# Optimization experiments

Measured on AMD Instinct MI355X. Metric: run time of the kernel, lower is better.

## Reference

```python
import jax, jax.numpy as jnp
import numpy as np

BN_EPS = 1e-5


def _bn_train(x, gamma, beta):
    # torch BatchNorm1d in training mode: normalize with batch mean and
    # biased batch variance.
    mu = jnp.mean(x, axis=0)
    var = jnp.var(x, axis=0)
    return (x - mu) * jax.lax.rsqrt(var + BN_EPS) * gamma + beta


def setup_inputs() -> dict:
    key = jax.random.key(0)
    ks = jax.random.split(key, 12)
    N, F_D, F_C, E, VOCAB, H = 16384, 26, 10, 16, 200000, 400
    D_IN = (F_D + F_C) * E  # 576
    return {
        "Xi_dense": jax.random.normal(ks[0], (N, F_D, 1), jnp.float32),
        "Xv": jax.random.uniform(ks[1], (N, F_D + F_C), jnp.float32),
        "Wd": jax.random.normal(ks[2], (F_D, E), jnp.float32) * 0.1,
        "bd": jax.random.normal(ks[3], (F_D, E), jnp.float32) * 0.1,
        "tables": jax.random.normal(ks[4], (F_C, VOCAB, E), jnp.float32) * 0.1,
        "W1": jax.random.normal(ks[5], (H, D_IN), jnp.float32) * 0.05,
        "b1": jax.random.normal(ks[6], (H,), jnp.float32) * 0.05,
        "g1": jnp.ones((H,), jnp.float32),
        "be1": jnp.zeros((H,), jnp.float32),
        "W2": jax.random.normal(ks[7], (H, H), jnp.float32) * 0.05,
        "b2": jax.random.normal(ks[8], (H,), jnp.float32) * 0.05,
        "g2": jnp.ones((H,), jnp.float32),
        "be2": jnp.zeros((H,), jnp.float32),
        "bias_vec": jax.random.normal(ks[9], (N,), jnp.float32),
        "Xi_cat": jax.random.randint(ks[10], (N, F_C, 1), 0, VOCAB, jnp.int32),
    }


def reference(Xi_dense, Xv, Wd, bd, tables, W1, b1, g1, be1,
              W2, b2, g2, be2, bias_vec, Xi_cat):
    N = Xi_dense.shape[0]
    # dense fields: per-field Linear(1, E) -> x * W + b, shape (N, 26, E)
    dense_emb = Xi_dense * Wd[None] + bd[None]  # (N,26,1)*(1,26,E) broadcast
    # categorical fields: per-field embedding lookup, shape (N, 10, E)
    cat_emb = jax.vmap(lambda tbl, idx: tbl[idx], in_axes=(0, 1), out_axes=1)(
        tables, Xi_cat[:, :, 0])
    # scale each field embedding by its Xv value
    all_emb = jnp.concatenate([dense_emb, cat_emb], axis=1) * Xv[:, :, None]  # (N,36,E)

    # fm first order: concat of all scaled field embeddings
    fm_first = all_emb.reshape(N, -1)  # (N, 576)
    # fm second order: 0.5 * ((sum)^2 - sum of squares)
    s = jnp.sum(all_emb, axis=1)                       # (N, E)
    fm_second = 0.5 * (s * s - jnp.sum(all_emb * all_emb, axis=1))  # (N, E)

    # deep part: Linear -> BatchNorm (train-mode stats) per hidden layer;
    # dropout p=0 -> identity.
    deep = fm_first
    deep = _bn_train(deep @ W1.T + b1, g1, be1)
    deep = _bn_train(deep @ W2.T + b2, g2, be2)

    total = (jnp.sum(fm_first, axis=1) + jnp.sum(fm_second, axis=1)
             + jnp.sum(deep, axis=1) + bias_vec)
    return total
```

## Files before the change

### kernel.cpp

```cpp
#include <hip/hip_runtime.h>

#define BN_EPS 1e-5f

typedef unsigned short u16;
typedef __attribute__((ext_vector_type(8))) short bf16x8;
typedef __attribute__((ext_vector_type(4))) float f32x4;

__device__ __forceinline__ u16 f2bf(float x) {
  union { float f; unsigned int u; } v; v.f = x;
  unsigned int r = v.u + 0x7fffu + ((v.u >> 16) & 1u);
  return (u16)(r >> 16);
}
__device__ __forceinline__ float bf2f(u16 h) {
  union { unsigned int u; float f; } v; v.u = ((unsigned int)h) << 16;
  return v.f;
}

__device__ __forceinline__ float wave_reduce_sum(float v) {
#pragma unroll
  for (int off = 1; off < 64; off <<= 1) v += __shfl_xor(v, off, 64);
  return v;
}

__device__ __forceinline__ void gload_lds16(const void* g, void* l) {
  __builtin_amdgcn_global_load_lds(
      (const __attribute__((address_space(1))) void*)g,
      (__attribute__((address_space(3))) void*)l, 16, 0, 0);
}

#define NBE 4096
__global__ __launch_bounds__(256) void embed_prep(
    const float* __restrict__ Xi_dense, const float* __restrict__ Xv,
    const float* __restrict__ Wd, const float* __restrict__ bd,
    const float* __restrict__ tables, const int* __restrict__ Xi_cat,
    const float* __restrict__ bias_vec, const float* __restrict__ W1,
    u16* __restrict__ fm_first, float* __restrict__ partial,
    u16* __restrict__ W1h) {
  const int t = threadIdx.x;
  if (blockIdx.x >= NBE) {
    const int base = (blockIdx.x - NBE) * 4096;
#pragma unroll
    for (int e = 0; e < 16; ++e) {
      const int idx = base + e * 256 + t;
      const int r = idx / 576;
      const int j = idx - r * 576;
      W1h[idx] = (r < 400) ? f2bf(W1[r * 576 + j]) : (u16)0;
    }
    return;
  }
  const int lane = t & 63;
  const int n = blockIdx.x * 4 + (t >> 6);

  const float* xv = Xv + n * 36;
  float sum_all = 0.f, s_e = 0.f, q_e = 0.f;

#pragma unroll
  for (int k = 0; k < 9; ++k) {
    const int idx = lane + 64 * k;
    const int f = idx >> 4;
    const int e = idx & 15;
    float val;
    if (f < 26) {
      val = Xi_dense[n * 26 + f] * Wd[f * 16 + e] + bd[f * 16 + e];
    } else {
      const int fc = f - 26;
      const int row = Xi_cat[n * 10 + fc];
      val = tables[(size_t)fc * 200000 * 16 + (size_t)row * 16 + e];
    }
    val *= xv[f];
    fm_first[(size_t)n * 576 + idx] = f2bf(val);
    sum_all += val;
    s_e += val;
    q_e += val * val;
  }

  float s_tot = s_e;
  s_tot += __shfl_xor(s_tot, 16, 64);
  s_tot += __shfl_xor(s_tot, 32, 64);
  float q_tot = q_e;
  q_tot += __shfl_xor(q_tot, 16, 64);
  q_tot += __shfl_xor(q_tot, 32, 64);

  const float fm2 = 0.5f * (s_tot * s_tot - q_tot);
  const float red1 = wave_reduce_sum(sum_all);
  const float red2 = wave_reduce_sum(fm2) * 0.25f;
  if (lane == 0) partial[n] = red1 + red2 + bias_vec[n];
}

template <int NFR>
__device__ __forceinline__ void gemm_body(
    const u16* __restrict__ A, int lda, const u16* __restrict__ W, int ldw,
    const float* __restrict__ bias, int nbias, u16* __restrict__ Y, int ldc,
    int Ncap, float* __restrict__ pS, float* __restrict__ pQ, int K, int nxb,
    int bx, int by, u16* As, u16* Bs, float (&rS)[2][4][2][16],
    float (&rQ)[2][4][2][16]) {
  const int t = threadIdx.x;
  const int bm = bx * 64;
  const int bn = by * 128;
  const int wid = t >> 6, lane = t & 63;
  const int wr = wid >> 1, wc = wid & 1;
  const int lr = lane & 15, lk = (lane >> 4) * 8;
  const int sr = lane >> 2;
  const int sk = (lane & 3) * 8;
  const bool active = (NFR == 4) || (wc == 0);

  f32x4 acc[2][NFR] = {};

  for (int kt = 0; kt < K; kt += 32) {
    gload_lds16(&A[(size_t)(bm + wid * 16 + sr) * lda + kt + sk],
                &As[wid * 512]);
#pragma unroll
    for (int i = 0; i < 2; ++i) {
      const int c = wid * 2 + i;
      if (NFR == 4 || c < 2)
        gload_lds16(&W[(size_t)(bn + c * 16 + sr) * ldw + kt + sk],
                    &Bs[c * 512]);
    }
    __syncthreads();

    if (active) {
      bf16x8 af[2], bfv[NFR];
#pragma unroll
      for (int mf = 0; mf < 2; ++mf)
        af[mf] = *(const bf16x8*)&As[(wr * 32 + mf * 16 + lr) * 32 + lk];
#pragma unroll
      for (int nf = 0; nf < NFR; ++nf)
        bfv[nf] = *(const bf16x8*)&Bs[(wc * 64 + nf * 16 + lr) * 32 + lk];
#pragma unroll
      for (int mf = 0; mf < 2; ++mf)
#pragma unroll
        for (int nf = 0; nf < NFR; ++nf)
          acc[mf][nf] = __builtin_amdgcn_mfma_f32_16x16x32_bf16(
              af[mf], bfv[nf], acc[mf][nf], 0, 0, 0);
    }
    __syncthreads();
  }

  const int l4 = (lane >> 4) * 4;
  if (active) {
#pragma unroll
    for (int nf = 0; nf < NFR; ++nf) {
      const int col = bn + wc * 64 + nf * 16 + lr;
      const float bb = (col < nbias) ? bias[col] : 0.f;
      float s = 0.f, q = 0.f;
#pragma unroll
      for (int mf = 0; mf < 2; ++mf) {
#pragma unroll
        for (int r = 0; r < 4; ++r) {
          const int row = bm + wr * 32 + mf * 16 + l4 + r;
          const float v = acc[mf][nf][r] + bb;
          s += v;
          q += v * v;
          if (col < Ncap) Y[(size_t)row * ldc + col] = f2bf(v);
        }
      }
      s += __shfl_xor(s, 16, 64);
      s += __shfl_xor(s, 32, 64);
      q += __shfl_xor(q, 16, 64);
      q += __shfl_xor(q, 32, 64);
      if (lane < 16) {
        rS[wc][nf][wr][lr] = s;
        rQ[wc][nf][wr][lr] = q;
      }
    }
  }
  __syncthreads();
  if (t < (NFR == 4 ? 128 : 32)) {
    const int wcc = t >> 6, nff = (t >> 4) & 3, c = t & 15;
    pS[(size_t)(bn + t) * nxb + bx] =
        rS[wcc][nff][0][c] + rS[wcc][nff][1][c];
    pQ[(size_t)(bn + t) * nxb + bx] =
        rQ[wcc][nff][0][c] + rQ[wcc][nff][1][c];
  }
}

__global__ __launch_bounds__(256) void gemm_bf16(
    const u16* __restrict__ A, int lda,
    const u16* __restrict__ W, int ldw,
    const float* __restrict__ bias, int nbias,
    u16* __restrict__ Y, int ldc, int Ncap,
    float* __restrict__ pS, float* __restrict__ pQ, int K, int nxb) {
  __shared__ u16 As[64 * 32];
  __shared__ u16 Bs[128 * 32];
  __shared__ float rS[2][4][2][16];
  __shared__ float rQ[2][4][2][16];
  const int bid = blockIdx.x;
  const int l = (bid & 7) * (gridDim.x >> 3) + (bid >> 3);
  const int bx = l >> 2, by = l & 3;
  if (by < 3)
    gemm_body<4>(A, lda, W, ldw, bias, nbias, Y, ldc, Ncap, pS, pQ, K, nxb,
                 bx, by, As, Bs, rS, rQ);
  else
    gemm_body<2>(A, lda, W, ldw, bias, nbias, Y, ldc, Ncap, pS, pQ, K, nxb,
                 bx, by, As, Bs, rS, rQ);
}

__global__ __launch_bounds__(256) void bn_ac(
    const float* __restrict__ pS, const float* __restrict__ pQ,
    const float* __restrict__ g, const float* __restrict__ be,
    float* __restrict__ a, float* __restrict__ c, int nxb) {
  const int wid = threadIdx.x >> 6, lane = threadIdx.x & 63;
  const int col = blockIdx.x * 4 + wid;
  float S = 0.f, Q = 0.f;
  for (int i = lane; i < nxb; i += 64) {
    S += pS[(size_t)col * nxb + i];
    Q += pQ[(size_t)col * nxb + i];
  }
#pragma unroll
  for (int off = 1; off < 64; off <<= 1) {
    S += __shfl_xor(S, off, 64);
    Q += __shfl_xor(Q, off, 64);
  }
  if (lane == 0) {
    const float mu = S * (1.f / 16384.f);
    const float var = Q * (1.f / 16384.f) - mu * mu;
    const float aa = g[col] * rsqrtf(var + BN_EPS);
    a[col] = aa;
    c[col] = be[col] - mu * aa;
  }
}

__global__ __launch_bounds__(256) void prep2(
    const float* __restrict__ a1, const float* __restrict__ c1,
    const float* __restrict__ W2, const float* __restrict__ b2,
    u16* __restrict__ W2p, float* __restrict__ b2p) {
  const int t = threadIdx.x;
  const int lane = t & 63;
  const int row = blockIdx.x * 4 + (t >> 6);
  const ushort4 z4 = {0, 0, 0, 0};
  if (row >= 400) {
    const int j1 = lane * 4;
    *(ushort4*)&W2p[(size_t)row * 416 + j1] = z4;
    const int j2 = 256 + lane * 4;
    if (j2 < 416) *(ushort4*)&W2p[(size_t)row * 416 + j2] = z4;
    if (lane == 0) b2p[row] = 0.f;
    return;
  }
  float dot = 0.f;
  {
    const int j = lane * 4;
    const float4 w = *(const float4*)&W2[(size_t)row * 400 + j];
    const float4 la = *(const float4*)&a1[j];
    const float4 lc = *(const float4*)&c1[j];
    ushort4 o = {f2bf(w.x * la.x), f2bf(w.y * la.y), f2bf(w.z * la.z),
                 f2bf(w.w * la.w)};
    *(ushort4*)&W2p[(size_t)row * 416 + j] = o;
    dot += w.x * lc.x + w.y * lc.y + w.z * lc.z + w.w * lc.w;
  }
  {
    const int j = 256 + lane * 4;
    if (j < 400) {
      const float4 w = *(const float4*)&W2[(size_t)row * 400 + j];
      const float4 la = *(const float4*)&a1[j];
      const float4 lc = *(const float4*)&c1[j];
      ushort4 o = {f2bf(w.x * la.x), f2bf(w.y * la.y), f2bf(w.z * la.z),
                   f2bf(w.w * la.w)};
      *(ushort4*)&W2p[(size_t)row * 416 + j] = o;
      dot += w.x * lc.x + w.y * lc.y + w.z * lc.z + w.w * lc.w;
    } else if (j < 416) {
      *(ushort4*)&W2p[(size_t)row * 416 + j] = z4;
    }
  }
  dot = wave_reduce_sum(dot);
  if (lane == 0) b2p[row] = b2[row] + dot;
}

__global__ __launch_bounds__(256) void final_kernel(
    const u16* __restrict__ Y2, const float* __restrict__ a2,
    const float* __restrict__ c2, const float* __restrict__ partial,
    float* __restrict__ out) {
  const int t = threadIdx.x;
  const int lane = t & 63;
  const int wid = t >> 6;
  const int j0 = lane * 8;
  float ar[8], cr[8];
  if (j0 < 400) {
    const float4 a0 = *(const float4*)&a2[j0];
    const float4 a1v = *(const float4*)&a2[j0 + 4];
    const float4 c0 = *(const float4*)&c2[j0];
    const float4 c1v = *(const float4*)&c2[j0 + 4];
    ar[0] = a0.x; ar[1] = a0.y; ar[2] = a0.z; ar[3] = a0.w;
    ar[4] = a1v.x; ar[5] = a1v.y; ar[6] = a1v.z; ar[7] = a1v.w;
    cr[0] = c0.x; cr[1] = c0.y; cr[2] = c0.z; cr[3] = c0.w;
    cr[4] = c1v.x; cr[5] = c1v.y; cr[6] = c1v.z; cr[7] = c1v.w;
  } else {
#pragma unroll
    for (int k = 0; k < 8; ++k) { ar[k] = 0.f; cr[k] = 0.f; }
  }
#pragma unroll
  for (int r = 0; r < 4; ++r) {
    const int n = blockIdx.x * 16 + wid * 4 + r;
    float acc = 0.f;
    if (j0 < 400) {
      const bf16x8 y = *(const bf16x8*)&Y2[(size_t)n * 400 + j0];
#pragma unroll
      for (int k = 0; k < 8; ++k)
        acc += fmaf(ar[k], bf2f((u16)y[k]), cr[k]);
    }
    acc = wave_reduce_sum(acc);
    if (lane == 0) out[n] = partial[n] + acc;
  }
}

extern "C" void kernel_launch(void* const* d_in, const int* in_sizes, int n_in,
                              void* d_out, int out_size, void* d_ws,
                              size_t ws_size, hipStream_t stream) {
  const float* Xi_dense = (const float*)d_in[0];
  const float* Xv = (const float*)d_in[1];
  const float* Wd = (const float*)d_in[2];
  const float* bd = (const float*)d_in[3];
  const float* tables = (const float*)d_in[4];
  const float* W1 = (const float*)d_in[5];
  const float* b1 = (const float*)d_in[6];
  const float* g1 = (const float*)d_in[7];
  const float* be1 = (const float*)d_in[8];
  const float* W2 = (const float*)d_in[9];
  const float* b2 = (const float*)d_in[10];
  const float* g2 = (const float*)d_in[11];
  const float* be2 = (const float*)d_in[12];
  const float* bias_vec = (const float*)d_in[13];
  const int* Xi_cat = (const int*)d_in[14];

  constexpr int N = 16384;
  constexpr int DIN = 576;
  constexpr int H = 400;
  constexpr int KP = 416;
  constexpr int WPAD = 512;
  constexpr int NXB = 256;

  u16* fm_first = (u16*)d_ws;
  u16* Y1h = fm_first + (size_t)N * DIN;
  u16* Y2h = Y1h + (size_t)N * KP;
  u16* W1h = Y2h + (size_t)N * H;
  u16* W2p = W1h + (size_t)WPAD * DIN;
  float* fptr = (float*)(W2p + (size_t)WPAD * KP);
  float* partial = fptr;
  float* pS = partial + N;
  float* pQ = pS + WPAD * NXB;
  float* a1 = pQ + WPAD * NXB;
  float* c1 = a1 + WPAD;
  float* a2 = c1 + WPAD;
  float* c2 = a2 + WPAD;
  float* b2p = c2 + WPAD;

  embed_prep<<<NBE + 72, 256, 0, stream>>>(Xi_dense, Xv, Wd, bd, tables,
                                           Xi_cat, bias_vec, W1, fm_first,
                                           partial, W1h);

  gemm_bf16<<<NXB * 4, 256, 0, stream>>>(fm_first, DIN, W1h, DIN, b1, H,
                                         Y1h, KP, KP, pS, pQ, DIN, NXB);

  bn_ac<<<100, 256, 0, stream>>>(pS, pQ, g1, be1, a1, c1, NXB);
  prep2<<<128, 256, 0, stream>>>(a1, c1, W2, b2, W2p, b2p);

  gemm_bf16<<<NXB * 4, 256, 0, stream>>>(Y1h, KP, W2p, KP, b2p, H,
                                         Y2h, H, H, pS, pQ, KP, NXB);

  bn_ac<<<100, 256, 0, stream>>>(pS, pQ, g2, be2, a2, c2, NXB);

  final_kernel<<<N / 16, 256, 0, stream>>>(Y2h, a2, c2, partial,
                                           (float*)d_out);
}
```

Baseline: 67.88 us.

## Double-buffer LDS in GEMM and enlarge M tile to 128 rows

The bf16 MFMA GEMM now uses double-buffered LDS tiles, loading the next K-slice while computing the current one, with one barrier per iteration instead of two. The M tile grows from 64 to 128 rows, so each wave computes 4 M fragments and the number of row blocks (NXB) halves. MFMA sections are wrapped in s_setprio to favour issue. The aim is to hide global-load latency and raise data reuse per block. The cost is more LDS and accumulator registers, which can lower occupancy, and half as many blocks in the grid.

```diff
diff --git a/kernel.cpp b/kernel.cpp
--- a/kernel.cpp
+++ b/kernel.cpp
@@ -92,10 +92,10 @@
     const u16* __restrict__ A, int lda, const u16* __restrict__ W, int ldw,
     const float* __restrict__ bias, int nbias, u16* __restrict__ Y, int ldc,
     int Ncap, float* __restrict__ pS, float* __restrict__ pQ, int K, int nxb,
-    int bx, int by, u16* As, u16* Bs, float (&rS)[2][4][2][16],
-    float (&rQ)[2][4][2][16]) {
+    int bx, int by, u16 (*As)[128 * 32], u16 (*Bs)[128 * 32],
+    float (&rS)[2][4][2][16], float (&rQ)[2][4][2][16]) {
   const int t = threadIdx.x;
-  const int bm = bx * 64;
+  const int bm = bx * 128;
   const int bn = by * 128;
   const int wid = t >> 6, lane = t & 63;
   const int wr = wid >> 1, wc = wid & 1;
@@ -104,37 +104,53 @@
   const int sk = (lane & 3) * 8;
   const bool active = (NFR == 4) || (wc == 0);
 
-  f32x4 acc[2][NFR] = {};
-
-  for (int kt = 0; kt < K; kt += 32) {
-    gload_lds16(&A[(size_t)(bm + wid * 16 + sr) * lda + kt + sk],
-                &As[wid * 512]);
+  f32x4 acc[4][NFR] = {};
+
+  auto STAGE = [&](int buf, int kt) {
 #pragma unroll
     for (int i = 0; i < 2; ++i) {
       const int c = wid * 2 + i;
+      gload_lds16(&A[(size_t)(bm + c * 16 + sr) * lda + kt + sk],
+                  &As[buf][c * 512]);
       if (NFR == 4 || c < 2)
         gload_lds16(&W[(size_t)(bn + c * 16 + sr) * ldw + kt + sk],
-                    &Bs[c * 512]);
-    }
-    __syncthreads();
-
+                    &Bs[buf][c * 512]);
+    }
+  };
+
+  auto COMPUTE = [&](int buf) {
     if (active) {
-      bf16x8 af[2], bfv[NFR];
-#pragma unroll
-      for (int mf = 0; mf < 2; ++mf)
-        af[mf] = *(const bf16x8*)&As[(wr * 32 + mf * 16 + lr) * 32 + lk];
+      bf16x8 af[4], bfv[NFR];
+#pragma unroll
+      for (int mf = 0; mf < 4; ++mf)
+        af[mf] = *(const bf16x8*)&As[buf][(wr * 64 + mf * 16 + lr) * 32 + lk];
 #pragma unroll
       for (int nf = 0; nf < NFR; ++nf)
-        bfv[nf] = *(const bf16x8*)&Bs[(wc * 64 + nf * 16 + lr) * 32 + lk];
-#pragma unroll
-      for (int mf = 0; mf < 2; ++mf)
+        bfv[nf] = *(const bf16x8*)&Bs[buf][(wc * 64 + nf * 16 + lr) * 32 + lk];
+      __builtin_amdgcn_s_setprio(1);
+#pragma unroll
+      for (int mf = 0; mf < 4; ++mf)
 #pragma unroll
         for (int nf = 0; nf < NFR; ++nf)
           acc[mf][nf] = __builtin_amdgcn_mfma_f32_16x16x32_bf16(
               af[mf], bfv[nf], acc[mf][nf], 0, 0, 0);
-    }
-    __syncthreads();
-  }
+      __builtin_amdgcn_s_setprio(0);
+    }
+  };
+
+  STAGE(0, 0);
+  asm volatile("s_waitcnt vmcnt(0)" ::: "memory");
+  __builtin_amdgcn_s_barrier();
+
+  int cur = 0;
+  for (int kt = 32; kt < K; kt += 32) {
+    STAGE(cur ^ 1, kt);
+    COMPUTE(cur);
+    asm volatile("s_waitcnt vmcnt(0)" ::: "memory");
+    __builtin_amdgcn_s_barrier();
+    cur ^= 1;
+  }
+  COMPUTE(cur);
 
   const int l4 = (lane >> 4) * 4;
   if (active) {
@@ -144,10 +160,10 @@
       const float bb = (col < nbias) ? bias[col] : 0.f;
       float s = 0.f, q = 0.f;
 #pragma unroll
-      for (int mf = 0; mf < 2; ++mf) {
+      for (int mf = 0; mf < 4; ++mf) {
 #pragma unroll
         for (int r = 0; r < 4; ++r) {
-          const int row = bm + wr * 32 + mf * 16 + l4 + r;
+          const int row = bm + wr * 64 + mf * 16 + l4 + r;
           const float v = acc[mf][nf][r] + bb;
           s += v;
           q += v * v;
@@ -180,8 +196,8 @@
     const float* __restrict__ bias, int nbias,
     u16* __restrict__ Y, int ldc, int Ncap,
     float* __restrict__ pS, float* __restrict__ pQ, int K, int nxb) {
-  __shared__ u16 As[64 * 32];
-  __shared__ u16 Bs[128 * 32];
+  __shared__ u16 As[2][128 * 32];
+  __shared__ u16 Bs[2][128 * 32];
   __shared__ float rS[2][4][2][16];
   __shared__ float rQ[2][4][2][16];
   const int bid = blockIdx.x;
@@ -326,7 +342,7 @@
   constexpr int H = 400;
   constexpr int KP = 416;
   constexpr int WPAD = 512;
-  constexpr int NXB = 256;
+  constexpr int NXB = 128;
 
   u16* fm_first = (u16*)d_ws;
   u16* Y1h = fm_first + (size_t)N * DIN;
```

After: 69.93 us. 3.0% more time.

## Fold BN stat reduction into GEMM atomics and restructure embedding kernel

Applied to the files above, without the earlier changes.

The GEMM epilogue now accumulates per-column sum and sum-of-squares with atomicAdd into zeroed buffers. This removes the two bn_ac kernels, and the BN affine coefficients are recomputed inline in prep2 and final_kernel. The embedding kernel is rewritten to process 64 rows per block, staging Xv, dense inputs, indices and Wd/bd in LDS. Each thread handles 8 contiguous elements with vector table loads and 16-byte bf16 stores. The atomics make the float summation order nondeterministic and add contention on 400 columns, and the zeroing depends on a single block of the embed kernel.

```diff
diff --git a/kernel.cpp b/kernel.cpp
--- a/kernel.cpp
+++ b/kernel.cpp
@@ -28,17 +28,21 @@
       (__attribute__((address_space(3))) void*)l, 16, 0, 0);
 }
 
-#define NBE 4096
 __global__ __launch_bounds__(256) void embed_prep(
     const float* __restrict__ Xi_dense, const float* __restrict__ Xv,
     const float* __restrict__ Wd, const float* __restrict__ bd,
     const float* __restrict__ tables, const int* __restrict__ Xi_cat,
     const float* __restrict__ bias_vec, const float* __restrict__ W1,
     u16* __restrict__ fm_first, float* __restrict__ partial,
-    u16* __restrict__ W1h) {
+    u16* __restrict__ W1h, float* __restrict__ statz) {
   const int t = threadIdx.x;
-  if (blockIdx.x >= NBE) {
-    const int base = (blockIdx.x - NBE) * 4096;
+  if (blockIdx.x >= 256) {
+    const int bb = blockIdx.x - 256;
+    if (bb == 0) {
+#pragma unroll
+      for (int i = 0; i < 8; ++i) statz[i * 256 + t] = 0.f;
+    }
+    const int base = bb * 4096;
 #pragma unroll
     for (int e = 0; e < 16; ++e) {
       const int idx = base + e * 256 + t;
@@ -48,50 +52,102 @@
     }
     return;
   }
-  const int lane = t & 63;
-  const int n = blockIdx.x * 4 + (t >> 6);
-
-  const float* xv = Xv + n * 36;
-  float sum_all = 0.f, s_e = 0.f, q_e = 0.f;
-
-#pragma unroll
-  for (int k = 0; k < 9; ++k) {
-    const int idx = lane + 64 * k;
-    const int f = idx >> 4;
-    const int e = idx & 15;
-    float val;
-    if (f < 26) {
-      val = Xi_dense[n * 26 + f] * Wd[f * 16 + e] + bd[f * 16 + e];
+
+  __shared__ float Xvs[64 * 37];
+  __shared__ float Xds[64 * 27];
+  __shared__ int Cis[64 * 11];
+  __shared__ float Wds[416], Bds[416];
+  const int n0 = blockIdx.x * 64;
+
+  for (int i = t; i < 2304; i += 256) {
+    const int r = i / 36;
+    Xvs[r * 37 + (i - r * 36)] = Xv[n0 * 36 + i];
+  }
+  for (int i = t; i < 1664; i += 256) {
+    const int r = i / 26;
+    Xds[r * 27 + (i - r * 26)] = Xi_dense[n0 * 26 + i];
+  }
+  for (int i = t; i < 640; i += 256) {
+    const int r = i / 10;
+    Cis[r * 11 + (i - r * 10)] = Xi_cat[n0 * 10 + i];
+  }
+  for (int i = t; i < 416; i += 256) {
+    Wds[i] = Wd[i];
+    Bds[i] = bd[i];
+  }
+  __syncthreads();
+
+  const int r = t >> 2, q = t & 3;
+  const int n = n0 + r;
+  const int fpar = q >> 1, eh = (q & 1) * 8;
+  float s8[8] = {}, q8[8] = {};
+  float sum_all = 0.f;
+  u16* frow = fm_first + (size_t)n * 576;
+
+#pragma unroll
+  for (int k = 0; k < 18; ++k) {
+    const int f = fpar + 2 * k;
+    const float xvv = Xvs[r * 37 + f];
+    float val[8];
+    if (k < 13) {
+      const float xd = Xds[r * 27 + f];
+      const float4 w0 = *(const float4*)&Wds[f * 16 + eh];
+      const float4 w1 = *(const float4*)&Wds[f * 16 + eh + 4];
+      const float4 b0 = *(const float4*)&Bds[f * 16 + eh];
+      const float4 b1 = *(const float4*)&Bds[f * 16 + eh + 4];
+      val[0] = fmaf(xd, w0.x, b0.x) * xvv;
+      val[1] = fmaf(xd, w0.y, b0.y) * xvv;
+      val[2] = fmaf(xd, w0.z, b0.z) * xvv;
+      val[3] = fmaf(xd, w0.w, b0.w) * xvv;
+      val[4] = fmaf(xd, w1.x, b1.x) * xvv;
+      val[5] = fmaf(xd, w1.y, b1.y) * xvv;
+      val[6] = fmaf(xd, w1.z, b1.z) * xvv;
+      val[7] = fmaf(xd, w1.w, b1.w) * xvv;
     } else {
       const int fc = f - 26;
-      const int row = Xi_cat[n * 10 + fc];
-      val = tables[(size_t)fc * 200000 * 16 + (size_t)row * 16 + e];
-    }
-    val *= xv[f];
-    fm_first[(size_t)n * 576 + idx] = f2bf(val);
-    sum_all += val;
-    s_e += val;
-    q_e += val * val;
-  }
-
-  float s_tot = s_e;
-  s_tot += __shfl_xor(s_tot, 16, 64);
-  s_tot += __shfl_xor(s_tot, 32, 64);
-  float q_tot = q_e;
-  q_tot += __shfl_xor(q_tot, 16, 64);
-  q_tot += __shfl_xor(q_tot, 32, 64);
-
-  const float fm2 = 0.5f * (s_tot * s_tot - q_tot);
-  const float red1 = wave_reduce_sum(sum_all);
-  const float red2 = wave_reduce_sum(fm2) * 0.25f;
-  if (lane == 0) partial[n] = red1 + red2 + bias_vec[n];
+      const int row = Cis[r * 11 + fc];
+      const float* tp =
+          tables + ((size_t)fc * 200000 + (size_t)row) * 16 + eh;
+      const float4 v0 = *(const float4*)tp;
+      const float4 v1 = *(const float4*)(tp + 4);
+      val[0] = v0.x * xvv;
+      val[1] = v0.y * xvv;
+      val[2] = v0.z * xvv;
+      val[3] = v0.w * xvv;
+      val[4] = v1.x * xvv;
+      val[5] = v1.y * xvv;
+      val[6] = v1.z * xvv;
+      val[7] = v1.w * xvv;
+    }
+    bf16x8 o;
+#pragma unroll
+    for (int j = 0; j < 8; ++j) {
+      s8[j] += val[j];
+      q8[j] += val[j] * val[j];
+      sum_all += val[j];
+      o[j] = (short)f2bf(val[j]);
+    }
+    *(bf16x8*)&frow[f * 16 + eh] = o;
+  }
+
+  float fm2h = 0.f;
+#pragma unroll
+  for (int j = 0; j < 8; ++j) {
+    const float se = s8[j] + __shfl_xor(s8[j], 2, 64);
+    const float qe = q8[j] + __shfl_xor(q8[j], 2, 64);
+    fm2h += se * se - qe;
+  }
+  const float fm2 = 0.5f * (fm2h + __shfl_xor(fm2h, 1, 64));
+  float srow = sum_all + __shfl_xor(sum_all, 1, 64);
+  srow += __shfl_xor(srow, 2, 64);
+  if (q == 0) partial[n] = srow + fm2 + bias_vec[n];
 }
 
 template <int NFR>
 __device__ __forceinline__ void gemm_body(
     const u16* __restrict__ A, int lda, const u16* __restrict__ W, int ldw,
     const float* __restrict__ bias, int nbias, u16* __restrict__ Y, int ldc,
-    int Ncap, float* __restrict__ pS, float* __restrict__ pQ, int K, int nxb,
+    int Ncap, float* __restrict__ aS, float* __restrict__ aQ, int K,
     int bx, int by, u16* As, u16* Bs, float (&rS)[2][4][2][16],
     float (&rQ)[2][4][2][16]) {
   const int t = threadIdx.x;
@@ -167,10 +223,8 @@
   __syncthreads();
   if (t < (NFR == 4 ? 128 : 32)) {
     const int wcc = t >> 6, nff = (t >> 4) & 3, c = t & 15;
-    pS[(size_t)(bn + t) * nxb + bx] =
-        rS[wcc][nff][0][c] + rS[wcc][nff][1][c];
-    pQ[(size_t)(bn + t) * nxb + bx] =
-        rQ[wcc][nff][0][c] + rQ[wcc][nff][1][c];
+    atomicAdd(&aS[bn + t], rS[wcc][nff][0][c] + rS[wcc][nff][1][c]);
+    atomicAdd(&aQ[bn + t], rQ[wcc][nff][0][c] + rQ[wcc][nff][1][c]);
   }
 }
 
@@ -179,7 +233,7 @@
     const u16* __restrict__ W, int ldw,
     const float* __restrict__ bias, int nbias,
     u16* __restrict__ Y, int ldc, int Ncap,
-    float* __restrict__ pS, float* __restrict__ pQ, int K, int nxb) {
+    float* __restrict__ aS, float* __restrict__ aQ, int K) {
   __shared__ u16 As[64 * 32];
   __shared__ u16 Bs[128 * 32];
   __shared__ float rS[2][4][2][16];
@@ -188,40 +242,35 @@
   const int l = (bid & 7) * (gridDim.x >> 3) + (bid >> 3);
   const int bx = l >> 2, by = l & 3;
   if (by < 3)
-    gemm_body<4>(A, lda, W, ldw, bias, nbias, Y, ldc, Ncap, pS, pQ, K, nxb,
+    gemm_body<4>(A, lda, W, ldw, bias, nbias, Y, ldc, Ncap, aS, aQ, K,
                  bx, by, As, Bs, rS, rQ);
   else
-    gemm_body<2>(A, lda, W, ldw, bias, nbias, Y, ldc, Ncap, pS, pQ, K, nxb,
+    gemm_body<2>(A, lda, W, ldw, bias, nbias, Y, ldc, Ncap, aS, aQ, K,
                  bx, by, As, Bs, rS, rQ);
 }
 
-__global__ __launch_bounds__(256) void bn_ac(
-    const float* __restrict__ pS, const float* __restrict__ pQ,
-    const float* __restrict__ g, const float* __restrict__ be,
-    float* __restrict__ a, float* __restrict__ c, int nxb) {
-  const int wid = threadIdx.x >> 6, lane = threadIdx.x & 63;
-  const int col = blockIdx.x * 4 + wid;
-  float S = 0.f, Q = 0.f;
-  for (int i = lane; i < nxb; i += 64) {
-    S += pS[(size_t)col * nxb + i];
-    Q += pQ[(size_t)col * nxb + i];
-  }
-#pragma unroll
-  for (int off = 1; off < 64; off <<= 1) {
-    S += __shfl_xor(S, off, 64);
-    Q += __shfl_xor(Q, off, 64);
-  }
-  if (lane == 0) {
-    const float mu = S * (1.f / 16384.f);
-    const float var = Q * (1.f / 16384.f) - mu * mu;
-    const float aa = g[col] * rsqrtf(var + BN_EPS);
-    a[col] = aa;
-    c[col] = be[col] - mu * aa;
-  }
+__device__ __forceinline__ void bn_affine4(const float* aS, const float* aQ,
+                                           const float* g, const float* be,
+                                           int j, float4& aa, float4& cc) {
+  const float4 S = *(const float4*)&aS[j];
+  const float4 Q = *(const float4*)&aQ[j];
+  const float4 G = *(const float4*)&g[j];
+  const float4 E = *(const float4*)&be[j];
+  const float inv = 1.f / 16384.f;
+  float mu, var;
+  mu = S.x * inv; var = Q.x * inv - mu * mu;
+  aa.x = G.x * rsqrtf(var + BN_EPS); cc.x = E.x - mu * aa.x;
+  mu = S.y * inv; var = Q.y * inv - mu * mu;
+  aa.y = G.y * rsqrtf(var + BN_EPS); cc.y = E.y - mu * aa.y;
+  mu = S.z * inv; var = Q.z * inv - mu * mu;
+  aa.z = G.z * rsqrtf(var + BN_EPS); cc.z = E.z - mu * aa.z;
+  mu = S.w * inv; var = Q.w * inv - mu * mu;
+  aa.w = G.w * rsqrtf(var + BN_EPS); cc.w = E.w - mu * aa.w;
 }
 
 __global__ __launch_bounds__(256) void prep2(
-    const float* __restrict__ a1, const float* __restrict__ c1,
+    const float* __restrict__ aS1, const float* __restrict__ aQ1,
+    const float* __restrict__ g1, const float* __restrict__ be1,
     const float* __restrict__ W2, const float* __restrict__ b2,
     u16* __restrict__ W2p, float* __restrict__ b2p) {
   const int t = threadIdx.x;
@@ -239,24 +288,24 @@
   float dot = 0.f;
   {
     const int j = lane * 4;
+    float4 aa, cc;
+    bn_affine4(aS1, aQ1, g1, be1, j, aa, cc);
     const float4 w = *(const float4*)&W2[(size_t)row * 400 + j];
-    const float4 la = *(const float4*)&a1[j];
-    const float4 lc = *(const float4*)&c1[j];
-    ushort4 o = {f2bf(w.x * la.x), f2bf(w.y * la.y), f2bf(w.z * la.z),
-                 f2bf(w.w * la.w)};
+    ushort4 o = {f2bf(w.x * aa.x), f2bf(w.y * aa.y), f2bf(w.z * aa.z),
+                 f2bf(w.w * aa.w)};
     *(ushort4*)&W2p[(size_t)row * 416 + j] = o;
-    dot += w.x * lc.x + w.y * lc.y + w.z * lc.z + w.w * lc.w;
+    dot += w.x * cc.x + w.y * cc.y + w.z * cc.z + w.w * cc.w;
   }
   {
     const int j = 256 + lane * 4;
     if (j < 400) {
+      float4 aa, cc;
+      bn_affine4(aS1, aQ1, g1, be1, j, aa, cc);
       const float4 w = *(const float4*)&W2[(size_t)row * 400 + j];
-      const float4 la = *(const float4*)&a1[j];
-      const float4 lc = *(const float4*)&c1[j];
-      ushort4 o = {f2bf(w.x * la.x), f2bf(w.y * la.y), f2bf(w.z * la.z),
-                   f2bf(w.w * la.w)};
+      ushort4 o = {f2bf(w.x * aa.x), f2bf(w.y * aa.y), f2bf(w.z * aa.z),
+                   f2bf(w.w * aa.w)};
       *(ushort4*)&W2p[(size_t)row * 416 + j] = o;
-      dot += w.x * lc.x + w.y * lc.y + w.z * lc.z + w.w * lc.w;
+      dot += w.x * cc.x + w.y * cc.y + w.z * cc.z + w.w * cc.w;
     } else if (j < 416) {
       *(ushort4*)&W2p[(size_t)row * 416 + j] = z4;
     }
@@ -266,8 +315,9 @@
 }
 
 __global__ __launch_bounds__(256) void final_kernel(
-    const u16* __restrict__ Y2, const float* __restrict__ a2,
-    const float* __restrict__ c2, const float* __restrict__ partial,
+    const u16* __restrict__ Y2, const float* __restrict__ aS2,
+    const float* __restrict__ aQ2, const float* __restrict__ g2,
+    const float* __restrict__ be2, const float* __restrict__ partial,
     float* __restrict__ out) {
   const int t = threadIdx.x;
   const int lane = t & 63;
@@ -275,14 +325,13 @@
   const int j0 = lane * 8;
   float ar[8], cr[8];
   if (j0 < 400) {
-    const float4 a0 = *(const float4*)&a2[j0];
-    const float4 a1v = *(const float4*)&a2[j0 + 4];
-    const float4 c0 = *(const float4*)&c2[j0];
-    const float4 c1v = *(const float4*)&c2[j0 + 4];
-    ar[0] = a0.x; ar[1] = a0.y; ar[2] = a0.z; ar[3] = a0.w;
-    ar[4] = a1v.x; ar[5] = a1v.y; ar[6] = a1v.z; ar[7] = a1v.w;
-    cr[0] = c0.x; cr[1] = c0.y; cr[2] = c0.z; cr[3] = c0.w;
-    cr[4] = c1v.x; cr[5] = c1v.y; cr[6] = c1v.z; cr[7] = c1v.w;
+    float4 aa0, cc0, aa1, cc1;
+    bn_affine4(aS2, aQ2, g2, be2, j0, aa0, cc0);
+    bn_affine4(aS2, aQ2, g2, be2, j0 + 4, aa1, cc1);
+    ar[0] = aa0.x; ar[1] = aa0.y; ar[2] = aa0.z; ar[3] = aa0.w;
+    ar[4] = aa1.x; ar[5] = aa1.y; ar[6] = aa1.z; ar[7] = aa1.w;
+    cr[0] = cc0.x; cr[1] = cc0.y; cr[2] = cc0.z; cr[3] = cc0.w;
+    cr[4] = cc1.x; cr[5] = cc1.y; cr[6] = cc1.z; cr[7] = cc1.w;
   } else {
 #pragma unroll
     for (int k = 0; k < 8; ++k) { ar[k] = 0.f; cr[k] = 0.f; }
@@ -335,29 +384,24 @@
   u16* W2p = W1h + (size_t)WPAD * DIN;
   float* fptr = (float*)(W2p + (size_t)WPAD * KP);
   float* partial = fptr;
-  float* pS = partial + N;
-  float* pQ = pS + WPAD * NXB;
-  float* a1 = pQ + WPAD * NXB;
-  float* c1 = a1 + WPAD;
-  float* a2 = c1 + WPAD;
-  float* c2 = a2 + WPAD;
-  float* b2p = c2 + WPAD;
-
-  embed_prep<<<NBE + 72, 256, 0, stream>>>(Xi_dense, Xv, Wd, bd, tables,
+  float* aS1 = partial + N;
+  float* aQ1 = aS1 + WPAD;
+  float* aS2 = aQ1 + WPAD;
+  float* aQ2 = aS2 + WPAD;
+  float* b2p = aQ2 + WPAD;
+
+  embed_prep<<<256 + 72, 256, 0, stream>>>(Xi_dense, Xv, Wd, bd, tables,
                                            Xi_cat, bias_vec, W1, fm_first,
-                                           partial, W1h);
+                                           partial, W1h, aS1);
 
   gemm_bf16<<<NXB * 4, 256, 0, stream>>>(fm_first, DIN, W1h, DIN, b1, H,
-                                         Y1h, KP, KP, pS, pQ, DIN, NXB);
-
-  bn_ac<<<100, 256, 0, stream>>>(pS, pQ, g1, be1, a1, c1, NXB);
-  prep2<<<128, 256, 0, stream>>>(a1, c1, W2, b2, W2p, b2p);
+                                         Y1h, KP, KP, aS1, aQ1, DIN);
+
+  prep2<<<128, 256, 0, stream>>>(aS1, aQ1, g1, be1, W2, b2, W2p, b2p);
 
   gemm_bf16<<<NXB * 4, 256, 0, stream>>>(Y1h, KP, W2p, KP, b2p, H,
-                                         Y2h, H, H, pS, pQ, KP, NXB);
-
-  bn_ac<<<100, 256, 0, stream>>>(pS, pQ, g2, be2, a2, c2, NXB);
-
-  final_kernel<<<N / 16, 256, 0, stream>>>(Y2h, a2, c2, partial,
+                                         Y2h, H, H, aS2, aQ2, KP);
+
+  final_kernel<<<N / 16, 256, 0, stream>>>(Y2h, aS2, aQ2, g2, be2, partial,
                                            (float*)d_out);
 }
```

Result: slower. 69.79 us (+2.8%).
